# Kernel optimization log

Measured on AMD Instinct MI355X. Metric: run time of the kernel, lower is better.

The kernel has to match this reference:

```python
import jax, jax.numpy as jnp
import numpy as np

N, NPG, BS = 32000, 1000, 32
E, H, L, R, K = 512000, 128, 3, 8, 64


def setup_inputs() -> dict:
    key = jax.random.key(0)
    ks = jax.random.split(key, 16)
    sc = 0.05
    x = jax.random.normal(ks[0], (N, H), jnp.float32)
    W_rel = jax.random.normal(ks[1], (L, R, H, H), jnp.float32) * sc
    W_self = jax.random.normal(ks[2], (L, H, H), jnp.float32) * sc
    rel_table = jax.random.normal(ks[3], (R, H), jnp.float32)
    Zn = jax.random.normal(ks[4], (K, H), jnp.float32) * sc
    proj_W = jax.random.normal(ks[5], (L * H, H), jnp.float32) * sc
    proj_b = jnp.zeros((H,), jnp.float32)
    fc_W = jax.random.normal(ks[6], (2 * L * H + 2 * H, 1), jnp.float32) * sc
    fc_b = jnp.zeros((1,), jnp.float32)
    rep_seq = jax.random.normal(ks[7], (BS, H), jnp.float32)
    src = jax.random.randint(ks[8], (E,), 0, N, jnp.int32)
    dst = jax.random.randint(ks[9], (E,), 0, N, jnp.int32)
    etype = jax.random.randint(ks[10], (E,), 0, R, jnp.int32)
    graph_id = (jnp.arange(N, dtype=jnp.int32) // NPG).astype(jnp.int32)
    head_ids = (jnp.arange(BS, dtype=jnp.int32) * NPG)           # node with id==1 per subgraph
    tail_ids = (jnp.arange(BS, dtype=jnp.int32) * NPG + 1)       # node with id==2 per subgraph
    rel_labels = jax.random.randint(ks[11], (BS,), 0, R, jnp.int32)
    return dict(x=x, W_rel=W_rel, W_self=W_self, rel_table=rel_table, Zn=Zn,
                proj_W=proj_W, proj_b=proj_b, fc_W=fc_W, fc_b=fc_b, rep_seq=rep_seq,
                src=src, dst=dst, etype=etype, graph_id=graph_id,
                head_ids=head_ids, tail_ids=tail_ids, rel_labels=rel_labels)


def reference(x, W_rel, W_self, rel_table, Zn, proj_W, proj_b, fc_W, fc_b, rep_seq,
              src, dst, etype, graph_id, head_ids, tail_ids, rel_labels):
    n, h_dim = x.shape
    bs = head_ids.shape[0]
    # RGCN message passing: aggregate src features per (dst, rel), then per-rel linear.
    seg = dst.astype(jnp.int32) * R + etype.astype(jnp.int32)  # [E]
    h = x
    reprs = []
    for l in range(L):
        agg = jax.ops.segment_sum(h[src], seg, num_segments=n * R)  # [N*R, H]
        agg = agg.reshape(n, R, h_dim)
        msg = jnp.einsum('nri,rio->no', agg, W_rel[l])
        h = jax.nn.relu(msg + h @ W_self[l])
        reprs.append(h)
    repr_ = jnp.stack(reprs, axis=1)  # [N, L, H]
    # mean_nodes pooling per subgraph
    counts = jax.ops.segment_sum(jnp.ones((n,), x.dtype), graph_id, num_segments=bs)
    g_mean = jax.ops.segment_sum(repr_, graph_id, num_segments=bs) / counts[:, None, None]
    g_out = jax.nn.leaky_relu(g_mean.reshape(bs, L * h_dim) @ proj_W + proj_b)  # [bs, H]
    # head/tail gathers
    head_flat = repr_[head_ids].reshape(bs, L * h_dim)
    tail_flat = repr_[tail_ids].reshape(bs, L * h_dim)
    rel_embs = rel_table[rel_labels]  # [bs, H]
    h_out = head_flat @ proj_W + proj_b
    t_out = tail_flat @ proj_W + proj_b
    # community view: cluster assignment (softmax) then summary (sigmoid)
    s1 = jax.nn.sigmoid(jax.nn.softmax(h_out @ Zn.T, axis=-1) @ Zn)
    s2 = jax.nn.sigmoid(jax.nn.softmax(t_out @ Zn.T, axis=-1) @ Zn)
    s = s1 * s2
    # view attention aggregation over [subgraph, sequence, community] views
    views = jnp.stack([g_out, rep_seq, s], axis=1)  # [bs, 3, H]
    att = jax.nn.softmax(jnp.sum(rel_embs[:, None, :] * views, axis=-1), axis=-1)  # [bs, 3]
    view_aggr = jnp.sum(att[:, :, None] * views, axis=1)  # [bs, H]
    # positive triplet scoring
    g_rep = jnp.concatenate([head_flat, tail_flat, rel_embs, view_aggr], axis=1)
    out_pos = g_rep @ fc_W + fc_b  # [bs, 1]
    return out_pos
```

## Files before the change

### kernel.cpp

```cpp
#include <hip/hip_runtime.h>

#define N_NODES 32000
#define NPG     1000
#define BSZ     32
#define NEDGE   512000
#define H       128
#define NL      3
#define NR      8
#define NW      1152
#define NBIN2   262144

typedef __attribute__((ext_vector_type(8))) short short8;
typedef __attribute__((ext_vector_type(4))) float float4v;

__device__ __forceinline__ float bf2f(unsigned short u) {
  union { unsigned int i; float f; } v;
  v.i = ((unsigned int)u) << 16;
  return v.f;
}
__device__ __forceinline__ unsigned short f2bf(float f) {
  union { float f; unsigned int i; } v;
  v.f = f;
  unsigned int x = v.i;
  return (unsigned short)((x + 0x7FFFu + ((x >> 16) & 1u)) >> 16);
}

__global__ __launch_bounds__(256) void k_prep(
    const float* __restrict__ x, const float* __restrict__ W_rel,
    const float* __restrict__ W_self, const int* __restrict__ dst,
    const int* __restrict__ graph_id,
    unsigned short* __restrict__ hb, unsigned short* __restrict__ Bt,
    int* __restrict__ cnt, int* __restrict__ gcount)
{
  const int b = blockIdx.x, t = threadIdx.x;
  if (b < 4000) {
    const size_t i = ((size_t)b * 256 + t) * 4;
    float4 v = *(const float4*)(x + i);
    ushort4 u = { f2bf(v.x), f2bf(v.y), f2bf(v.z), f2bf(v.w) };
    *(ushort4*)(hb + i) = u;
  } else if (b < 5728) {
    const int g = (b - 4000) * 256 + t;
    const int k = g & 127;
    const int n = (g >> 7) % NW;
    const int l = g / (NW * H);
    float v = (n < 1024) ? W_rel[(((size_t)l * NR + (n >> 7)) * H + k) * H + (n & 127)]
                         : W_self[((size_t)l * H + k) * H + (n - 1024)];
    Bt[(size_t)l * (NW * H) + (size_t)n * H + k] = f2bf(v);
  } else if (b < 7728) {
    const int bb = b - 5728;
    const int e = bb * 256 + t;
    atomicAdd(&cnt[dst[e] * 8 + (bb & 7)], 1);
  } else {
    __shared__ int hist[BSZ];
    if (t < BSZ) hist[t] = 0;
    __syncthreads();
    const int n = (b - 7728) * 256 + t;
    if (n < N_NODES) atomicAdd(&hist[graph_id[n]], 1);
    __syncthreads();
    if (t < BSZ) { int v = hist[t]; if (v) atomicAdd(&gcount[t], v); }
  }
}

__global__ __launch_bounds__(256) void k_scanA(const int* __restrict__ cnt,
                                               int* __restrict__ bsum) {
  __shared__ int red[256];
  const int t = threadIdx.x;
  int4 v = *(const int4*)(cnt + blockIdx.x * 1024 + t * 4);
  red[t] = v.x + v.y + v.z + v.w;
  __syncthreads();
  for (int off = 128; off > 0; off >>= 1) {
    if (t < off) red[t] += red[t + off];
    __syncthreads();
  }
  if (t == 0) bsum[blockIdx.x] = red[0];
}

__global__ __launch_bounds__(256) void k_scanB(const int* __restrict__ bsum,
                                               int* __restrict__ boff) {
  __shared__ int v[256];
  const int t = threadIdx.x;
  v[t] = bsum[t];
  __syncthreads();
  if (t == 0) {
    int r = 0;
    for (int i = 0; i < 256; ++i) { int c = v[i]; v[i] = r; r += c; }
  }
  __syncthreads();
  boff[t] = v[t];
}

__global__ __launch_bounds__(256) void k_scanC(const int* __restrict__ cnt,
                                               const int* __restrict__ boff,
                                               int* __restrict__ row_ptr2,
                                               int* __restrict__ cursor) {
  __shared__ int ts[256];
  const int t = threadIdx.x;
  const int base = blockIdx.x * 1024 + t * 4;
  int4 v = *(const int4*)(cnt + base);
  const int s = v.x + v.y + v.z + v.w;
  ts[t] = s;
  __syncthreads();
  for (int off = 1; off < 256; off <<= 1) {
    int val = (t >= off) ? ts[t - off] : 0;
    __syncthreads();
    ts[t] += val;
    __syncthreads();
  }
  int ex = ts[t] - s + boff[blockIdx.x];
  int4 w = { ex, ex + v.x, ex + v.x + v.y, ex + v.x + v.y + v.z };
  *(int4*)(row_ptr2 + base) = w;
  *(int4*)(cursor + base) = w;
}

__global__ void k_fill(const int* __restrict__ src, const int* __restrict__ dst,
                       const int* __restrict__ etype, int* __restrict__ cursor,
                       int* __restrict__ edge_off) {
  int e = blockIdx.x * blockDim.x + threadIdx.x;
  if (e < NEDGE) {
    int p = atomicAdd(&cursor[dst[e] * 8 + (blockIdx.x & 7)], 1);
    edge_off[p] = src[e] * NW + etype[e] * H;
  }
}

__global__ __launch_bounds__(256) void k_gemm9(
    const unsigned short* __restrict__ Ah,
    const unsigned short* __restrict__ Bt,
    unsigned short* __restrict__ G)
{
  __shared__ unsigned short lds_a[128 * 136];
  __shared__ unsigned short lds_b[128 * 136];
  const int tid  = threadIdx.x;
  const int wave = tid >> 6, lane = tid & 63;
  const int l15 = lane & 15, quad = lane >> 4;
  const int m0 = blockIdx.x * 128;
  const int n0 = blockIdx.y * 128;
  const int mb = (wave & 1) * 64;
  const int nb = (wave >> 1) * 64;

  #pragma unroll
  for (int s = 0; s < 8; ++s) {
    int f  = s * 256 + tid;
    int m  = f >> 4;
    int ko = (f & 15) * 8;
    *(uint4*)(lds_a + m * 136 + ko) = *(const uint4*)(Ah + (size_t)(m0 + m) * H + ko);
    *(uint4*)(lds_b + m * 136 + ko) = *(const uint4*)(Bt + (size_t)(n0 + m) * H + ko);
  }
  __syncthreads();

  float4v acc[4][4];
  #pragma unroll
  for (int i = 0; i < 4; ++i)
    #pragma unroll
    for (int j = 0; j < 4; ++j) acc[i][j] = (float4v){0.f, 0.f, 0.f, 0.f};

  #pragma unroll
  for (int ks = 0; ks < 4; ++ks) {
    const int ko = ks * 32 + quad * 8;
    short8 afr[4], bfr[4];
    #pragma unroll
    for (int i = 0; i < 4; ++i)
      afr[i] = *(const short8*)(lds_a + (mb + i * 16 + l15) * 136 + ko);
    #pragma unroll
    for (int j = 0; j < 4; ++j)
      bfr[j] = *(const short8*)(lds_b + (nb + j * 16 + l15) * 136 + ko);
    #pragma unroll
    for (int i = 0; i < 4; ++i)
      #pragma unroll
      for (int j = 0; j < 4; ++j)
        acc[i][j] = __builtin_amdgcn_mfma_f32_16x16x32_bf16(afr[i], bfr[j], acc[i][j], 0, 0, 0);
  }

  __syncthreads();
  #pragma unroll
  for (int i = 0; i < 4; ++i)
    #pragma unroll
    for (int j = 0; j < 4; ++j)
      #pragma unroll
      for (int r = 0; r < 4; ++r)
        lds_a[(mb + i * 16 + quad * 4 + r) * 136 + nb + j * 16 + l15] = f2bf(acc[i][j][r]);
  __syncthreads();
  #pragma unroll
  for (int s = 0; s < 8; ++s) {
    int f  = s * 256 + tid;
    int m  = f >> 4;
    int ko = (f & 15) * 8;
    *(uint4*)(G + (size_t)(m0 + m) * NW + n0 + ko) = *(const uint4*)(lds_a + m * 136 + ko);
  }
}

__global__ __launch_bounds__(256) void k_gather(
    const unsigned short* __restrict__ G, const int* __restrict__ row_ptr2,
    const int* __restrict__ edge_off, unsigned short* __restrict__ Hnext)
{
  const int node = blockIdx.x * 4 + (threadIdx.x >> 6);
  const int lane = threadIdx.x & 63;
  const int half = lane >> 5;
  const int li   = lane & 31;
  const int c0   = li * 4;
  const int beg = row_ptr2[node << 3];
  const int end = row_ptr2[(node << 3) + 8];
  float s0 = 0.f, s1 = 0.f, s2 = 0.f, s3 = 0.f;
  if (half == 0) {
    uint2 u = *(const uint2*)(G + (size_t)node * NW + 1024 + c0);
    s0 = bf2f((unsigned short)(u.x & 0xffff));
    s1 = bf2f((unsigned short)(u.x >> 16));
    s2 = bf2f((unsigned short)(u.y & 0xffff));
    s3 = bf2f((unsigned short)(u.y >> 16));
  }
#define ACC4(u) { \
    s0 += bf2f((unsigned short)((u).x & 0xffff)); \
    s1 += bf2f((unsigned short)((u).x >> 16));    \
    s2 += bf2f((unsigned short)((u).y & 0xffff)); \
    s3 += bf2f((unsigned short)((u).y >> 16)); }
  int e = beg + half;
  for (; e + 6 < end; e += 8) {
    int o0 = edge_off[e],     o1 = edge_off[e + 2];
    int o2 = edge_off[e + 4], o3 = edge_off[e + 6];
    uint2 u0 = *(const uint2*)(G + o0 + c0);
    uint2 u1 = *(const uint2*)(G + o1 + c0);
    uint2 u2 = *(const uint2*)(G + o2 + c0);
    uint2 u3 = *(const uint2*)(G + o3 + c0);
    ACC4(u0) ACC4(u1) ACC4(u2) ACC4(u3)
  }
  for (; e < end; e += 2) {
    int o = edge_off[e];
    uint2 u = *(const uint2*)(G + o + c0);
    ACC4(u)
  }
#undef ACC4
  s0 += __shfl_xor(s0, 32);
  s1 += __shfl_xor(s1, 32);
  s2 += __shfl_xor(s2, 32);
  s3 += __shfl_xor(s3, 32);
  if (half == 0) {
    uint2 w;
    w.x = (unsigned int)f2bf(fmaxf(s0, 0.f)) | ((unsigned int)f2bf(fmaxf(s1, 0.f)) << 16);
    w.y = (unsigned int)f2bf(fmaxf(s2, 0.f)) | ((unsigned int)f2bf(fmaxf(s3, 0.f)) << 16);
    *(uint2*)(Hnext + (size_t)node * H + c0) = w;
  }
}

__global__ void k_gmean(const unsigned short* __restrict__ hb, float* __restrict__ gmean)
{
  const int g = blockIdx.x, l = blockIdx.y, c = blockIdx.z, t = threadIdx.x;
  const unsigned short* base =
      hb + ((size_t)(l + 1) * N_NODES + (size_t)g * NPG + (size_t)c * (NPG / 8)) * H + t * 2;
  float sx = 0.f, sy = 0.f;
  for (int i = 0; i < 125; ++i) {
    unsigned int u = *(const unsigned int*)(base + (size_t)i * H);
    sx += bf2f((unsigned short)(u & 0xffff));
    sy += bf2f((unsigned short)(u >> 16));
  }
  float* gp = gmean + (size_t)g * (NL * H) + l * H + t * 2;
  atomicAdd(gp, sx);
  atomicAdd(gp + 1, sy);
}

__global__ __launch_bounds__(128) void k_final(
    const unsigned short* __restrict__ hb, const float* __restrict__ gmean,
    const int* __restrict__ gcount,
    const float* __restrict__ rel_tb, const float* __restrict__ Zn,
    const float* __restrict__ projW, const float* __restrict__ projB,
    const float* __restrict__ fcW, const float* __restrict__ fcB,
    const float* __restrict__ repSeq,
    const int* __restrict__ head_ids, const int* __restrict__ tail_ids,
    const int* __restrict__ rel_lab, float* __restrict__ out)
{
  const int b = blockIdx.x;
  const int o = threadIdx.x;
  __shared__ float gm[384], hf[384], tf[384];
  __shared__ float go[128], ho[128], t_o[128], re[128], rs[128], sv[128];
  __shared__ float lg[128], pr[128], red[128], att[3];

  const int hid = head_ids[b], tlid = tail_ids[b], rl = rel_lab[b];
  const float cinv = 1.f / (float)gcount[b];
  #pragma unroll
  for (int l = 0; l < NL; ++l) {
    gm[l * H + o] = gmean[(size_t)b * (NL * H) + l * H + o] * cinv;
    hf[l * H + o] = bf2f(hb[((size_t)(l + 1) * N_NODES + hid) * H + o]);
    tf[l * H + o] = bf2f(hb[((size_t)(l + 1) * N_NODES + tlid) * H + o]);
  }
  re[o] = rel_tb[rl * H + o];
  rs[o] = repSeq[b * H + o];
  __syncthreads();

  float pb = projB[o];
  float sg = pb, sh = pb, st = pb;
  for (int i = 0; i < NL * H; ++i) {
    float wv = projW[i * H + o];
    sg = fmaf(gm[i], wv, sg);
    sh = fmaf(hf[i], wv, sh);
    st = fmaf(tf[i], wv, st);
  }
  go[o] = (sg > 0.f) ? sg : 0.01f * sg;
  ho[o] = sh;
  t_o[o] = st;
  __syncthreads();

  {
    const int k = o & 63;
    const float* v = (o < 64) ? ho : t_o;
    float s = 0.f;
    for (int i = 0; i < H; ++i) s = fmaf(v[i], Zn[k * H + i], s);
    lg[o] = s;
  }
  __syncthreads();
  if (o < 2) {
    float* l0 = &lg[o * 64];
    float* p0 = &pr[o * 64];
    float mx = l0[0];
    for (int k = 1; k < 64; ++k) mx = fmaxf(mx, l0[k]);
    float sum = 0.f;
    for (int k = 0; k < 64; ++k) { float e = __expf(l0[k] - mx); p0[k] = e; sum += e; }
    float inv = 1.f / sum;
    for (int k = 0; k < 64; ++k) p0[k] *= inv;
  }
  __syncthreads();
  {
    float s1 = 0.f, s2 = 0.f;
    for (int k = 0; k < 64; ++k) {
      float z = Zn[k * H + o];
      s1 = fmaf(pr[k], z, s1);
      s2 = fmaf(pr[64 + k], z, s2);
    }
    s1 = 1.f / (1.f + __expf(-s1));
    s2 = 1.f / (1.f + __expf(-s2));
    sv[o] = s1 * s2;
  }
  __syncthreads();
  if (o == 0) {
    float d0 = 0.f, d1 = 0.f, d2 = 0.f;
    for (int i = 0; i < H; ++i) { d0 += re[i] * go[i]; d1 += re[i] * rs[i]; d2 += re[i] * sv[i]; }
    float mx = fmaxf(d0, fmaxf(d1, d2));
    float e0 = __expf(d0 - mx), e1 = __expf(d1 - mx), e2 = __expf(d2 - mx);
    float inv = 1.f / (e0 + e1 + e2);
    att[0] = e0 * inv; att[1] = e1 * inv; att[2] = e2 * inv;
  }
  __syncthreads();
  float va = att[0] * go[o] + att[1] * rs[o] + att[2] * sv[o];

  float p = 0.f;
  p = fmaf(hf[o],       fcW[o],       p);
  p = fmaf(hf[128 + o], fcW[128 + o], p);
  p = fmaf(hf[256 + o], fcW[256 + o], p);
  p = fmaf(tf[o],       fcW[384 + o], p);
  p = fmaf(tf[128 + o], fcW[512 + o], p);
  p = fmaf(tf[256 + o], fcW[640 + o], p);
  p = fmaf(re[o],       fcW[768 + o], p);
  p = fmaf(va,          fcW[896 + o], p);
  red[o] = p;
  __syncthreads();
  if (o == 0) {
    float s = 0.f;
    for (int i = 0; i < 128; ++i) s += red[i];
    out[b] = s + fcB[0];
  }
}

extern "C" void kernel_launch(void* const* d_in, const int* in_sizes, int n_in,
                              void* d_out, int out_size, void* d_ws, size_t ws_size,
                              hipStream_t stream) {
  const float* x        = (const float*)d_in[0];
  const float* W_rel    = (const float*)d_in[1];
  const float* W_self   = (const float*)d_in[2];
  const float* rel_tb   = (const float*)d_in[3];
  const float* Zn       = (const float*)d_in[4];
  const float* proj_W   = (const float*)d_in[5];
  const float* proj_b   = (const float*)d_in[6];
  const float* fc_W     = (const float*)d_in[7];
  const float* fc_b     = (const float*)d_in[8];
  const float* rep_seq  = (const float*)d_in[9];
  const int* src      = (const int*)d_in[10];
  const int* dst      = (const int*)d_in[11];
  const int* etype    = (const int*)d_in[12];
  const int* graph_id = (const int*)d_in[13];
  const int* head_ids = (const int*)d_in[14];
  const int* tail_ids = (const int*)d_in[15];
  const int* rel_lab  = (const int*)d_in[16];
  float* out = (float*)d_out;

  char* w = (char*)d_ws;
  unsigned short* G  = (unsigned short*)w; w += (size_t)N_NODES * NW * 2;
  unsigned short* hb = (unsigned short*)w; w += (size_t)(NL + 1) * N_NODES * H * 2;
  unsigned short* Bt = (unsigned short*)w; w += (size_t)NL * NW * H * 2;
  int* row_ptr2 = (int*)w;  w += (size_t)(NBIN2 + 8) * 4;
  int* cursor   = (int*)w;  w += (size_t)NBIN2 * 4;
  int* edge_off = (int*)w;  w += (size_t)NEDGE * 4;
  int* bsum     = (int*)w;  w += (size_t)256 * 4;
  int* boff     = (int*)w;  w += (size_t)256 * 4;
  char* z = w;
  int* cnt     = (int*)w;   w += (size_t)NBIN2 * 4;
  int* gcount  = (int*)w;   w += (size_t)32 * 4;
  float* gmean = (float*)w; w += (size_t)BSZ * NL * H * 4;
  size_t zbytes = (size_t)(w - z);

  hipMemsetAsync(z, 0, zbytes, stream);
  k_prep <<<7853, 256, 0, stream>>>(x, W_rel, W_self, dst, graph_id, hb, Bt, cnt, gcount);
  k_scanA<<<NBIN2 / 1024, 256, 0, stream>>>(cnt, bsum);
  k_scanB<<<1, 256, 0, stream>>>(bsum, boff);
  k_scanC<<<NBIN2 / 1024, 256, 0, stream>>>(cnt, boff, row_ptr2, cursor);
  k_fill <<<NEDGE / 256, 256, 0, stream>>>(src, dst, etype, cursor, edge_off);

  for (int l = 0; l < NL; ++l) {
    const unsigned short* hp = hb + (size_t)l * N_NODES * H;
    unsigned short* hn = hb + (size_t)(l + 1) * N_NODES * H;
    k_gemm9 <<<dim3(N_NODES / 128, 9), 256, 0, stream>>>(hp, Bt + (size_t)l * NW * H, G);
    k_gather<<<N_NODES / 4, 256, 0, stream>>>(G, row_ptr2, edge_off, hn);
  }
  k_gmean<<<dim3(BSZ, NL, 8), 64, 0, stream>>>(hb, gmean);
  k_final<<<BSZ, H, 0, stream>>>(hb, gmean, gcount, rel_tb, Zn, proj_W, proj_b, fc_W, fc_b,
                                 rep_seq, head_ids, tail_ids, rel_lab, out);
  (void)in_sizes; (void)n_in; (void)out_size; (void)ws_size;
}
```

Before: 342.6 us.

## Fuse scan passes, swizzle GEMM LDS with direct loads, fold graph mean into gather

Merges the single-block scanB into scanC: every scanC block now redundantly scans the 256 block sums itself. The GEMM tile loads go through global_load_lds into an XOR-swizzled, unpadded LDS layout instead of register-staged copies into a padded layout. The per-graph mean reduction moves into the gather kernel's epilogue as block-level partial sums with atomics, which drops the separate gmean kernel and its re-read of the hidden states. This removes two launches and some memory traffic, at the cost of more atomics and a redundant scan in each block.

```diff
diff --git a/kernel.cpp b/kernel.cpp
--- a/kernel.cpp
+++ b/kernel.cpp
@@ -23,6 +23,12 @@
   v.f = f;
   unsigned int x = v.i;
   return (unsigned short)((x + 0x7FFFu + ((x >> 16) & 1u)) >> 16);
+}
+
+__device__ __forceinline__ void gl_lds16(const void* g, void* l) {
+  __builtin_amdgcn_global_load_lds((__attribute__((address_space(1))) void*)g,
+                                   (__attribute__((address_space(3))) void*)l,
+                                   16, 0, 0);
 }
 
 __global__ __launch_bounds__(256) void k_prep(
@@ -75,38 +81,27 @@
   if (t == 0) bsum[blockIdx.x] = red[0];
 }
 
-__global__ __launch_bounds__(256) void k_scanB(const int* __restrict__ bsum,
-                                               int* __restrict__ boff) {
-  __shared__ int v[256];
-  const int t = threadIdx.x;
-  v[t] = bsum[t];
-  __syncthreads();
-  if (t == 0) {
-    int r = 0;
-    for (int i = 0; i < 256; ++i) { int c = v[i]; v[i] = r; r += c; }
-  }
-  __syncthreads();
-  boff[t] = v[t];
-}
-
 __global__ __launch_bounds__(256) void k_scanC(const int* __restrict__ cnt,
-                                               const int* __restrict__ boff,
+                                               const int* __restrict__ bsum,
                                                int* __restrict__ row_ptr2,
                                                int* __restrict__ cursor) {
-  __shared__ int ts[256];
+  __shared__ int ts[256], bsx[256];
   const int t = threadIdx.x;
   const int base = blockIdx.x * 1024 + t * 4;
   int4 v = *(const int4*)(cnt + base);
   const int s = v.x + v.y + v.z + v.w;
-  ts[t] = s;
+  ts[t]  = s;
+  bsx[t] = bsum[t];
   __syncthreads();
   for (int off = 1; off < 256; off <<= 1) {
-    int val = (t >= off) ? ts[t - off] : 0;
+    int a = (t >= off) ? ts[t - off]  : 0;
+    int c = (t >= off) ? bsx[t - off] : 0;
     __syncthreads();
-    ts[t] += val;
+    ts[t] += a; bsx[t] += c;
     __syncthreads();
   }
-  int ex = ts[t] - s + boff[blockIdx.x];
+  const int boff = (blockIdx.x == 0) ? 0 : bsx[blockIdx.x - 1];
+  int ex = ts[t] - s + boff;
   int4 w = { ex, ex + v.x, ex + v.x + v.y, ex + v.x + v.y + v.z };
   *(int4*)(row_ptr2 + base) = w;
   *(int4*)(cursor + base) = w;
@@ -127,8 +122,8 @@
     const unsigned short* __restrict__ Bt,
     unsigned short* __restrict__ G)
 {
-  __shared__ unsigned short lds_a[128 * 136];
-  __shared__ unsigned short lds_b[128 * 136];
+  __shared__ __align__(16) unsigned short lds_a[128 * 128];
+  __shared__ __align__(16) unsigned short lds_b[128 * 128];
   const int tid  = threadIdx.x;
   const int wave = tid >> 6, lane = tid & 63;
   const int l15 = lane & 15, quad = lane >> 4;
@@ -138,12 +133,13 @@
   const int nb = (wave >> 1) * 64;
 
   #pragma unroll
-  for (int s = 0; s < 8; ++s) {
-    int f  = s * 256 + tid;
-    int m  = f >> 4;
-    int ko = (f & 15) * 8;
-    *(uint4*)(lds_a + m * 136 + ko) = *(const uint4*)(Ah + (size_t)(m0 + m) * H + ko);
-    *(uint4*)(lds_b + m * 136 + ko) = *(const uint4*)(Bt + (size_t)(n0 + m) * H + ko);
+  for (int i = 0; i < 8; ++i) {
+    const int g  = (i * 4 + wave) * 64 + lane;
+    const int m  = g >> 4;
+    const int cr = g & 15;
+    const int cs = cr ^ (m & 7);
+    gl_lds16(Ah + (size_t)(m0 + m) * H + cs * 8, lds_a + (size_t)g * 8);
+    gl_lds16(Bt + (size_t)(n0 + m) * H + cs * 8, lds_b + (size_t)g * 8);
   }
   __syncthreads();
 
@@ -155,14 +151,18 @@
 
   #pragma unroll
   for (int ks = 0; ks < 4; ++ks) {
-    const int ko = ks * 32 + quad * 8;
+    const int cr = ks * 4 + quad;
     short8 afr[4], bfr[4];
     #pragma unroll
-    for (int i = 0; i < 4; ++i)
-      afr[i] = *(const short8*)(lds_a + (mb + i * 16 + l15) * 136 + ko);
+    for (int i = 0; i < 4; ++i) {
+      const int row = mb + i * 16 + l15;
+      afr[i] = *(const short8*)(lds_a + row * H + ((cr ^ (row & 7)) * 8));
+    }
     #pragma unroll
-    for (int j = 0; j < 4; ++j)
-      bfr[j] = *(const short8*)(lds_b + (nb + j * 16 + l15) * 136 + ko);
+    for (int j = 0; j < 4; ++j) {
+      const int row = nb + j * 16 + l15;
+      bfr[j] = *(const short8*)(lds_b + row * H + ((cr ^ (row & 7)) * 8));
+    }
     #pragma unroll
     for (int i = 0; i < 4; ++i)
       #pragma unroll
@@ -176,23 +176,30 @@
     #pragma unroll
     for (int j = 0; j < 4; ++j)
       #pragma unroll
-      for (int r = 0; r < 4; ++r)
-        lds_a[(mb + i * 16 + quad * 4 + r) * 136 + nb + j * 16 + l15] = f2bf(acc[i][j][r]);
+      for (int r = 0; r < 4; ++r) {
+        const int row = mb + i * 16 + quad * 4 + r;
+        const int col = nb + j * 16 + l15;
+        lds_a[row * H + ((((col >> 3) ^ (row & 7)) << 3) | (col & 7))] = f2bf(acc[i][j][r]);
+      }
   __syncthreads();
   #pragma unroll
   for (int s = 0; s < 8; ++s) {
-    int f  = s * 256 + tid;
-    int m  = f >> 4;
-    int ko = (f & 15) * 8;
-    *(uint4*)(G + (size_t)(m0 + m) * NW + n0 + ko) = *(const uint4*)(lds_a + m * 136 + ko);
+    const int g  = s * 256 + tid;
+    const int m  = g >> 4;
+    const int cr = g & 15;
+    *(uint4*)(G + (size_t)(m0 + m) * NW + n0 + cr * 8) =
+        *(const uint4*)(lds_a + m * H + ((cr ^ (m & 7)) * 8));
   }
 }
 
 __global__ __launch_bounds__(256) void k_gather(
     const unsigned short* __restrict__ G, const int* __restrict__ row_ptr2,
-    const int* __restrict__ edge_off, unsigned short* __restrict__ Hnext)
+    const int* __restrict__ edge_off, unsigned short* __restrict__ Hnext,
+    float* __restrict__ gmean, int layer)
 {
-  const int node = blockIdx.x * 4 + (threadIdx.x >> 6);
+  __shared__ float gsum[4][128];
+  const int wv   = threadIdx.x >> 6;
+  const int node = blockIdx.x * 4 + wv;
   const int lane = threadIdx.x & 63;
   const int half = lane >> 5;
   const int li   = lane & 31;
@@ -232,28 +239,24 @@
   s1 += __shfl_xor(s1, 32);
   s2 += __shfl_xor(s2, 32);
   s3 += __shfl_xor(s3, 32);
+  const float r0 = fmaxf(s0, 0.f), r1 = fmaxf(s1, 0.f);
+  const float r2 = fmaxf(s2, 0.f), r3 = fmaxf(s3, 0.f);
   if (half == 0) {
     uint2 w;
-    w.x = (unsigned int)f2bf(fmaxf(s0, 0.f)) | ((unsigned int)f2bf(fmaxf(s1, 0.f)) << 16);
-    w.y = (unsigned int)f2bf(fmaxf(s2, 0.f)) | ((unsigned int)f2bf(fmaxf(s3, 0.f)) << 16);
+    w.x = (unsigned int)f2bf(r0) | ((unsigned int)f2bf(r1) << 16);
+    w.y = (unsigned int)f2bf(r2) | ((unsigned int)f2bf(r3) << 16);
     *(uint2*)(Hnext + (size_t)node * H + c0) = w;
-  }
-}
-
-__global__ void k_gmean(const unsigned short* __restrict__ hb, float* __restrict__ gmean)
-{
-  const int g = blockIdx.x, l = blockIdx.y, c = blockIdx.z, t = threadIdx.x;
-  const unsigned short* base =
-      hb + ((size_t)(l + 1) * N_NODES + (size_t)g * NPG + (size_t)c * (NPG / 8)) * H + t * 2;
-  float sx = 0.f, sy = 0.f;
-  for (int i = 0; i < 125; ++i) {
-    unsigned int u = *(const unsigned int*)(base + (size_t)i * H);
-    sx += bf2f((unsigned short)(u & 0xffff));
-    sy += bf2f((unsigned short)(u >> 16));
-  }
-  float* gp = gmean + (size_t)g * (NL * H) + l * H + t * 2;
-  atomicAdd(gp, sx);
-  atomicAdd(gp + 1, sy);
+    gsum[wv][c0]     = r0;
+    gsum[wv][c0 + 1] = r1;
+    gsum[wv][c0 + 2] = r2;
+    gsum[wv][c0 + 3] = r3;
+  }
+  __syncthreads();
+  const int t = threadIdx.x;
+  if (t < 128) {
+    float v = gsum[0][t] + gsum[1][t] + gsum[2][t] + gsum[3][t];
+    atomicAdd(&gmean[(size_t)(blockIdx.x / 250) * (NL * H) + layer * H + t], v);
+  }
 }
 
 __global__ __launch_bounds__(128) void k_final(
@@ -387,7 +390,6 @@
   int* cursor   = (int*)w;  w += (size_t)NBIN2 * 4;
   int* edge_off = (int*)w;  w += (size_t)NEDGE * 4;
   int* bsum     = (int*)w;  w += (size_t)256 * 4;
-  int* boff     = (int*)w;  w += (size_t)256 * 4;
   char* z = w;
   int* cnt     = (int*)w;   w += (size_t)NBIN2 * 4;
   int* gcount  = (int*)w;   w += (size_t)32 * 4;
@@ -397,17 +399,15 @@
   hipMemsetAsync(z, 0, zbytes, stream);
   k_prep <<<7853, 256, 0, stream>>>(x, W_rel, W_self, dst, graph_id, hb, Bt, cnt, gcount);
   k_scanA<<<NBIN2 / 1024, 256, 0, stream>>>(cnt, bsum);
-  k_scanB<<<1, 256, 0, stream>>>(bsum, boff);
-  k_scanC<<<NBIN2 / 1024, 256, 0, stream>>>(cnt, boff, row_ptr2, cursor);
+  k_scanC<<<NBIN2 / 1024, 256, 0, stream>>>(cnt, bsum, row_ptr2, cursor);
   k_fill <<<NEDGE / 256, 256, 0, stream>>>(src, dst, etype, cursor, edge_off);
 
   for (int l = 0; l < NL; ++l) {
     const unsigned short* hp = hb + (size_t)l * N_NODES * H;
     unsigned short* hn = hb + (size_t)(l + 1) * N_NODES * H;
     k_gemm9 <<<dim3(N_NODES / 128, 9), 256, 0, stream>>>(hp, Bt + (size_t)l * NW * H, G);
-    k_gather<<<N_NODES / 4, 256, 0, stream>>>(G, row_ptr2, edge_off, hn);
-  }
-  k_gmean<<<dim3(BSZ, NL, 8), 64, 0, stream>>>(hb, gmean);
+    k_gather<<<N_NODES / 4, 256, 0, stream>>>(G, row_ptr2, edge_off, hn, gmean, l);
+  }
   k_final<<<BSZ, H, 0, stream>>>(hb, gmean, gcount, rel_tb, Zn, proj_W, proj_b, fc_W, fc_b,
                                  rep_seq, head_ids, tail_ids, rel_lab, out);
   (void)in_sizes; (void)n_in; (void)out_size; (void)ws_size;
```

New measurement: 388.3 us. 13.3% more time.
